# Optimization experiments

Measured on AMD Instinct MI355X. Metric: run time of the kernel, lower is better.

## Reference

```python
import jax, jax.numpy as jnp
import numpy as np

N_NODES = 50000
N_EDGES = 150000
D_FEAT = 512
HIDDEN = 512
N_CLASSES = 47


def gcn_conv(x, edge_index, W, b, n_nodes):
    """PyG GCNConv: out = D^{-1/2} (A + I) D^{-1/2} (x @ W) + b."""
    h = x @ W  # [N, out_dim] dense GEMM
    loop = jnp.arange(n_nodes, dtype=edge_index.dtype)
    row = jnp.concatenate([edge_index[0], loop])  # source
    col = jnp.concatenate([edge_index[1], loop])  # target
    ones = jnp.ones(row.shape[0], dtype=h.dtype)
    deg = jax.ops.segment_sum(ones, col, num_segments=n_nodes)  # in-degree + 1
    dinv = jnp.where(deg > 0, jax.lax.rsqrt(deg), 0.0)
    norm = dinv[row] * dinv[col]  # [E+N]
    msg = norm[:, None] * h[row]  # gather + scale
    out = jax.ops.segment_sum(msg, col, num_segments=n_nodes)  # scatter-add
    return out + b


def setup_inputs() -> dict:
    key = jax.random.key(0)
    k1, k2, k3, k4, k5, k6 = jax.random.split(key, 6)
    x = jax.random.normal(k1, (N_NODES, D_FEAT), dtype=jnp.float32)
    edge_index = jax.random.randint(k2, (2, N_EDGES), 0, N_NODES, dtype=jnp.int64)
    s1 = (6.0 / (D_FEAT + HIDDEN)) ** 0.5
    s2 = (6.0 / (HIDDEN + N_CLASSES)) ** 0.5
    W1 = jax.random.uniform(k3, (D_FEAT, HIDDEN), jnp.float32, -s1, s1)
    b1 = jnp.zeros((HIDDEN,), jnp.float32)
    W2 = jax.random.uniform(k4, (HIDDEN, N_CLASSES), jnp.float32, -s2, s2)
    b2 = jnp.zeros((N_CLASSES,), jnp.float32)
    return {"x": x, "edge_index": edge_index, "W1": W1, "b1": b1, "W2": W2, "b2": b2}


def reference(x, edge_index, W1, b1, W2, b2):
    n = x.shape[0]
    h = gcn_conv(x, edge_index, W1, b1, n)
    h = jax.nn.relu(h)
    # F.dropout(p=0.5, training=self.training): eval mode -> identity
    out = gcn_conv(h, edge_index, W2, b2, n)
    return out
```

## Files before the change

kernel.cpp:

```cpp
#include <hip/hip_runtime.h>
#include <hip/hip_bf16.h>

#define NNODES 50000
#define NEDGES 150000
#define DFEAT  512
#define HID    512
#define NCLS   47
#define ELLW   32

typedef __hip_bfloat16 bf16;
typedef __attribute__((ext_vector_type(8))) short short8;
typedef __attribute__((ext_vector_type(4))) float float4v;

typedef const __attribute__((address_space(1))) unsigned int* gas_t;
typedef __attribute__((address_space(3))) unsigned int* las_t;
__device__ __forceinline__ void load_lds16(const void* g, void* l) {
    __builtin_amdgcn_global_load_lds((gas_t)g, (las_t)l, 16, 0, 0);
}

__device__ __forceinline__ float bfbits_lo(unsigned int w) {
    return __uint_as_float((w & 0xFFFFu) << 16);
}
__device__ __forceinline__ float bfbits_hi(unsigned int w) {
    return __uint_as_float(w & 0xFFFF0000u);
}

__device__ __forceinline__ int eidx(const void* ei, int half, int e, int is64) {
    if (is64) return (int)((const long long*)ei)[(size_t)half * NEDGES + e];
    return ((const int*)ei)[half * NEDGES + e];
}

#define ZB ((NNODES + 255) / 256)
#define NZH2 ((NNODES * 64 / 4 + 255) / 256)
#define PR_ZH2 (1 + ZB)
#define PR_W1T (PR_ZH2 + NZH2)
#define PR_B1  (PR_W1T + 1024)
#define PR_W2T (PR_B1 + 2)
#define PR_B2  (PR_W2T + 128)
#define PR_GRID (PR_B2 + 1)

__global__ __launch_bounds__(256) void k_prep0(
    const void* x, const void* ei, const void* W1, const void* b1,
    const void* W2, const void* b2, int* flags, unsigned int* cnt,
    bf16* W1T, float* b1c, bf16* W2T, float* b2c, float* h2) {
    __shared__ int sh[128];
    __shared__ int shflag;
    const int b = blockIdx.x, t = threadIdx.x;

    if (b >= 1 && b < 1 + ZB) {
        int i = (b - 1) * 256 + t;
        if (i < NNODES) cnt[i] = 0u;
        return;
    }
    if (b >= PR_ZH2 && b < PR_W1T) {
        int i = (b - PR_ZH2) * 256 + t;
        if (i < NNODES * 64 / 4)
            ((float4v*)h2)[i] = (float4v){0.f, 0.f, 0.f, 0.f};
        return;
    }

    if (t < 64) {
        const unsigned short* xs = (const unsigned short*)x;
        int c = 0;
        for (int i = t; i < 256; i += 64) {
            unsigned int e = (xs[2 * i] >> 7) & 0xFF;
            c += (e >= 117 && e <= 130) ? 1 : 0;
        }
        sh[t] = c;
        if (b == 0) {
            const int* w = (const int*)ei;
            int o = 0;
            for (int i = 2 * t + 1; i < 512; i += 128) o |= w[i];
            sh[64 + t] = o;
        }
    }
    __syncthreads();
    if (t == 0) {
        int C = 0;
        for (int i = 0; i < 64; i++) C += sh[i];
        shflag = (C > 128) ? 1 : 0;
        if (b == 0) {
            int O = 0;
            for (int i = 0; i < 64; i++) O |= sh[64 + i];
            flags[0] = shflag;
            flags[1] = (O == 0) ? 1 : 0;
        }
    }
    __syncthreads();
    const int isb = shflag;

    if (b == 0) return;

    if (b >= PR_W1T && b < PR_B1) {
        int i = (b - PR_W1T) * 256 + t;
        int k = i / HID, n = i % HID;
        float v = isb ? __bfloat162float(((const bf16*)W1)[i]) : ((const float*)W1)[i];
        W1T[(size_t)n * DFEAT + k] = __float2bfloat16(v);
    } else if (b >= PR_B1 && b < PR_W2T) {
        int i = (b - PR_B1) * 256 + t;
        if (i < HID)
            b1c[i] = isb ? __bfloat162float(((const bf16*)b1)[i]) : ((const float*)b1)[i];
    } else if (b >= PR_W2T && b < PR_B2) {
        int i = (b - PR_W2T) * 256 + t;
        int n = i / HID, k = i % HID;
        float v = 0.0f;
        if (n < NCLS) {
            size_t idx = (size_t)k * NCLS + n;
            v = isb ? __bfloat162float(((const bf16*)W2)[idx]) : ((const float*)W2)[idx];
        }
        W2T[(size_t)n * HID + k] = __float2bfloat16(v);
    } else if (b == PR_B2) {
        if (t < 64)
            b2c[t] = (t < NCLS)
                ? (isb ? __bfloat162float(((const bf16*)b2)[t]) : ((const float*)b2)[t])
                : 0.0f;
    }
}

__global__ void k_fill_ell(const void* ei, int* cnt, int* ell, const int* flags) {
    int e = blockIdx.x * blockDim.x + threadIdx.x;
    if (e >= NEDGES) return;
    int is64 = flags[1];
    int v = eidx(ei, 1, e, is64);
    int u = eidx(ei, 0, e, is64);
    int slot = atomicAdd(&cnt[v], 1);
    if (slot < ELLW) ell[v * ELLW + slot] = u;
}

__global__ __launch_bounds__(256) void k_aggx(const void* __restrict__ X,
                                              const int* __restrict__ cnt,
                                              const int* __restrict__ ell,
                                              bf16* __restrict__ ax,
                                              const int* __restrict__ flags) {
    int v = blockIdx.x * 4 + (threadIdx.x >> 6);
    int lane = threadIdx.x & 63;
    if (v >= NNODES) return;
    int d8 = lane * 8;
    int degr = cnt[v];
    int deg = degr < ELLW ? degr : ELLW;
    float dv = rsqrtf(1.0f + (float)degr);
    float s2 = dv * dv;
    const int* er = ell + (size_t)v * ELLW;
    float a0, a1, a2, a3, a4, a5, a6, a7;
    if (flags[0]) {
        const bf16* xb = (const bf16*)X;
        uint4 w = *(const uint4*)(xb + (size_t)v * 512 + d8);
        a0 = s2 * bfbits_lo(w.x); a1 = s2 * bfbits_hi(w.x);
        a2 = s2 * bfbits_lo(w.y); a3 = s2 * bfbits_hi(w.y);
        a4 = s2 * bfbits_lo(w.z); a5 = s2 * bfbits_hi(w.z);
        a6 = s2 * bfbits_lo(w.w); a7 = s2 * bfbits_hi(w.w);
        for (int p = 0; p < deg; p += 8) {
            int u[8]; float nw[8];
#pragma unroll
            for (int c = 0; c < 8; ++c) {
                int jp = (p + c < deg) ? p + c : p;
                u[c] = er[jp];
            }
#pragma unroll
            for (int c = 0; c < 8; ++c)
                nw[c] = (p + c < deg) ? rsqrtf(1.0f + (float)cnt[u[c]]) * dv : 0.f;
#pragma unroll
            for (int c = 0; c < 8; ++c) {
                uint4 q = *(const uint4*)(xb + (size_t)u[c] * 512 + d8);
                float nwc = nw[c];
                a0 += nwc * bfbits_lo(q.x); a1 += nwc * bfbits_hi(q.x);
                a2 += nwc * bfbits_lo(q.y); a3 += nwc * bfbits_hi(q.y);
                a4 += nwc * bfbits_lo(q.z); a5 += nwc * bfbits_hi(q.z);
                a6 += nwc * bfbits_lo(q.w); a7 += nwc * bfbits_hi(q.w);
            }
        }
    } else {
        const float* xf = (const float*)X;
        const float* p0 = xf + (size_t)v * 512 + d8;
        float4v f0 = *(const float4v*)p0, f1 = *(const float4v*)(p0 + 4);
        a0 = s2 * f0[0]; a1 = s2 * f0[1]; a2 = s2 * f0[2]; a3 = s2 * f0[3];
        a4 = s2 * f1[0]; a5 = s2 * f1[1]; a6 = s2 * f1[2]; a7 = s2 * f1[3];
        for (int p = 0; p < deg; ++p) {
            int u = er[p];
            float nw = rsqrtf(1.0f + (float)cnt[u]) * dv;
            const float* pu = xf + (size_t)u * 512 + d8;
            float4v g0 = *(const float4v*)pu, g1 = *(const float4v*)(pu + 4);
            a0 += nw * g0[0]; a1 += nw * g0[1]; a2 += nw * g0[2]; a3 += nw * g0[3];
            a4 += nw * g1[0]; a5 += nw * g1[1]; a6 += nw * g1[2]; a7 += nw * g1[3];
        }
    }
    bf16 o[8];
    o[0] = __float2bfloat16(a0); o[1] = __float2bfloat16(a1);
    o[2] = __float2bfloat16(a2); o[3] = __float2bfloat16(a3);
    o[4] = __float2bfloat16(a4); o[5] = __float2bfloat16(a5);
    o[6] = __float2bfloat16(a6); o[7] = __float2bfloat16(a7);
    *(uint4*)(ax + (size_t)v * 512 + d8) = *(uint4*)o;
}

__global__ __launch_bounds__(256, 4) void k_fgemm64(
    const bf16* __restrict__ ax, const bf16* __restrict__ W1T,
    const float* __restrict__ b1c, const bf16* __restrict__ W2T,
    float* __restrict__ h2, int rows_per_xcd, int n_row_tiles) {
    const int b = blockIdx.x;
    const int xcd = b & 7;
    const int s = b >> 3;
    const int col_t = s & 3;
    const int lr = s >> 2;
    const int row_t = xcd * rows_per_xcd + lr;
    if (row_t >= n_row_tiles) return;

    __shared__ bf16 smem[12288];
    bf16* As = smem;
    bf16* Bs = smem + 4096;
    const int tid = threadIdx.x;
    const int wave = tid >> 6, lane = tid & 63;
    const int row0 = row_t * 64;
    const int gc0 = col_t * 128;

    const int rb16 = wave * 16;
    const int frow = lane & 15;
    const int fk = lane >> 4;

    float4v acc[8];
#pragma unroll
    for (int j = 0; j < 8; j++) acc[j] = (float4v){0.f, 0.f, 0.f, 0.f};

    for (int k0 = 0; k0 < DFEAT; k0 += 64) {
        __syncthreads();
#pragma unroll
        for (int t = 0; t < 2; ++t) {
            int g8 = wave * 2 + t;
            int r = g8 * 8 + (lane >> 3);
            int gr = row0 + r; if (gr >= NNODES) gr = NNODES - 1;
            int ck = (lane & 7) ^ (r & 7);
            load_lds16(ax + (size_t)gr * DFEAT + k0 + ck * 8, &As[g8 * 8 * 64]);
        }
#pragma unroll
        for (int t = 0; t < 4; ++t) {
            int g8 = wave * 4 + t;
            int cl = g8 * 8 + (lane >> 3);
            int ck = (lane & 7) ^ (cl & 7);
            load_lds16(W1T + (size_t)(gc0 + cl) * DFEAT + k0 + ck * 8, &Bs[g8 * 8 * 64]);
        }
        __syncthreads();
#pragma unroll
        for (int ki = 0; ki < 2; ++ki) {
            const int cc = ki * 4 + fk;
            int r = rb16 + frow;
            short8 a = *(const short8*)&As[r * 64 + (cc ^ (r & 7)) * 8];
            short8 b8[8];
#pragma unroll
            for (int j = 0; j < 8; j++) {
                int cl = j * 16 + frow;
                b8[j] = *(const short8*)&Bs[cl * 64 + (cc ^ (cl & 7)) * 8];
            }
#pragma unroll
            for (int j = 0; j < 8; j++)
                acc[j] = __builtin_amdgcn_mfma_f32_16x16x32_bf16(a, b8[j], acc[j], 0, 0, 0);
        }
    }

    __syncthreads();
    {
        float bias[8];
#pragma unroll
        for (int j = 0; j < 8; j++) bias[j] = b1c[gc0 + j * 16 + frow];
#pragma unroll
        for (int r = 0; r < 4; r++) {
            int row = rb16 + fk * 4 + r;
#pragma unroll
            for (int j = 0; j < 8; j++) {
                int col = j * 16 + frow;
                float v = acc[j][r] + bias[j];
                v = v > 0.f ? v : 0.f;
                int ck2 = (col >> 3) ^ (row & 7);
                smem[row * 128 + ck2 * 8 + (col & 7)] = __float2bfloat16(v);
            }
        }
    }
    __syncthreads();

    float4v acc2[4];
#pragma unroll
    for (int j = 0; j < 4; j++) acc2[j] = (float4v){0.f, 0.f, 0.f, 0.f};
#pragma unroll
    for (int ks = 0; ks < 4; ++ks) {
        const int kk = ks * 32 + fk * 8;
        const int p = kk >> 3;
        int row = rb16 + frow;
        short8 a2 = *(const short8*)&smem[row * 128 + ((p ^ (row & 7)) * 8)];
        short8 b2f[4];
#pragma unroll
        for (int j = 0; j < 4; j++) {
            int n = j * 16 + frow;
            b2f[j] = *(const short8*)(W2T + (size_t)n * HID + gc0 + kk);
        }
#pragma unroll
        for (int j = 0; j < 4; j++)
            acc2[j] = __builtin_amdgcn_mfma_f32_16x16x32_bf16(a2, b2f[j], acc2[j], 0, 0, 0);
    }

#pragma unroll
    for (int r = 0; r < 4; r++) {
        int grow = row0 + rb16 + fk * 4 + r;
        if (grow < NNODES) {
#pragma unroll
            for (int j = 0; j < 4; j++)
                atomicAdd(&h2[(size_t)grow * 64 + j * 16 + frow], acc2[j][r]);
        }
    }
}

__global__ __launch_bounds__(256) void k_agg2(const float* __restrict__ h2,
                                              const int* __restrict__ cnt,
                                              const int* __restrict__ ell,
                                              const float* __restrict__ b2c,
                                              void* out, const int* flags) {
    int v = blockIdx.x * 16 + (threadIdx.x >> 4);
    int l = threadIdx.x & 15;
    if (v >= NNODES) return;
    int d4 = l * 4;
    int degr = cnt[v];
    int deg = degr < ELLW ? degr : ELLW;
    float dv = rsqrtf(1.0f + (float)degr);
    const int* er = ell + (size_t)v * ELLW;
    float4v w = *(const float4v*)(h2 + (size_t)v * 64 + d4);
    float s2 = dv * dv;
    float a0 = s2 * w[0], a1 = s2 * w[1], a2 = s2 * w[2], a3 = s2 * w[3];
    for (int p = 0; p < deg; p += 4) {
        int u0 = er[p];
        int u1 = er[(p + 1 < deg) ? p + 1 : p];
        int u2 = er[(p + 2 < deg) ? p + 2 : p];
        int u3 = er[(p + 3 < deg) ? p + 3 : p];
        float nw0 = rsqrtf(1.0f + (float)cnt[u0]) * dv;
        float nw1 = (p + 1 < deg) ? rsqrtf(1.0f + (float)cnt[u1]) * dv : 0.f;
        float nw2 = (p + 2 < deg) ? rsqrtf(1.0f + (float)cnt[u2]) * dv : 0.f;
        float nw3 = (p + 3 < deg) ? rsqrtf(1.0f + (float)cnt[u3]) * dv : 0.f;
        float4v q0 = *(const float4v*)(h2 + (size_t)u0 * 64 + d4);
        float4v q1 = *(const float4v*)(h2 + (size_t)u1 * 64 + d4);
        float4v q2 = *(const float4v*)(h2 + (size_t)u2 * 64 + d4);
        float4v q3 = *(const float4v*)(h2 + (size_t)u3 * 64 + d4);
        a0 += nw0 * q0[0] + nw1 * q1[0] + nw2 * q2[0] + nw3 * q3[0];
        a1 += nw0 * q0[1] + nw1 * q1[1] + nw2 * q2[1] + nw3 * q3[1];
        a2 += nw0 * q0[2] + nw1 * q1[2] + nw2 * q2[2] + nw3 * q3[2];
        a3 += nw0 * q0[3] + nw1 * q1[3] + nw2 * q2[3] + nw3 * q3[3];
    }
    a0 += b2c[d4 + 0]; a1 += b2c[d4 + 1]; a2 += b2c[d4 + 2]; a3 += b2c[d4 + 3];
    size_t base = (size_t)v * NCLS;
    if (flags[0]) {
        bf16* ob = (bf16*)out;
        if (d4 + 0 < NCLS) ob[base + d4 + 0] = __float2bfloat16(a0);
        if (d4 + 1 < NCLS) ob[base + d4 + 1] = __float2bfloat16(a1);
        if (d4 + 2 < NCLS) ob[base + d4 + 2] = __float2bfloat16(a2);
        if (d4 + 3 < NCLS) ob[base + d4 + 3] = __float2bfloat16(a3);
    } else {
        float* of = (float*)out;
        if (d4 + 0 < NCLS) of[base + d4 + 0] = a0;
        if (d4 + 1 < NCLS) of[base + d4 + 1] = a1;
        if (d4 + 2 < NCLS) of[base + d4 + 2] = a2;
        if (d4 + 3 < NCLS) of[base + d4 + 3] = a3;
    }
}

extern "C" void kernel_launch(void* const* d_in, const int* in_sizes, int n_in,
                              void* d_out, int out_size, void* d_ws, size_t ws_size,
                              hipStream_t stream) {
    const void* x  = d_in[0];
    const void* ei = d_in[1];
    const void* W1 = d_in[2];
    const void* b1 = d_in[3];
    const void* W2 = d_in[4];
    const void* b2 = d_in[5];

    char* base = (char*)d_ws;
    auto alloc = [&](size_t bytes) -> char* {
        char* p = base;
        base += (bytes + 255) & ~(size_t)255;
        return p;
    };
    int*   flags  = (int*)alloc(64);
    int*   cnt    = (int*)alloc(sizeof(int) * NNODES);
    int*   ell    = (int*)alloc(sizeof(int) * (size_t)NNODES * ELLW);
    bf16*  W1T    = (bf16*)alloc(sizeof(bf16) * DFEAT * HID);
    float* b1c    = (float*)alloc(sizeof(float) * HID);
    bf16*  W2T    = (bf16*)alloc(sizeof(bf16) * 64 * HID);
    float* b2c    = (float*)alloc(sizeof(float) * 64);
    float* h2     = (float*)alloc(sizeof(float) * (size_t)NNODES * 64);
    bf16*  ax     = (bf16*)alloc(sizeof(bf16) * (size_t)NNODES * DFEAT);

    k_prep0<<<PR_GRID, 256, 0, stream>>>(x, ei, W1, b1, W2, b2, flags,
                                         (unsigned int*)cnt, W1T, b1c, W2T, b2c, h2);
    k_fill_ell<<<(NEDGES + 255) / 256, 256, 0, stream>>>(ei, cnt, ell, flags);
    k_aggx<<<(NNODES + 3) / 4, 256, 0, stream>>>(x, cnt, ell, ax, flags);
    const int rowblocks = (NNODES + 63) / 64;
    const int rows_per_xcd = (rowblocks + 7) / 8;
    k_fgemm64<<<8 * rows_per_xcd * 4, 256, 0, stream>>>(ax, W1T, b1c, W2T, h2,
                                                        rows_per_xcd, rowblocks);
    k_agg2<<<(NNODES + 15) / 16, 256, 0, stream>>>(h2, cnt, ell, b2c, d_out, flags);
}
```

Before: 297.4 us.

## Compute full hidden width per block and store h2 directly, dropping atomics and zeroing

The fused GEMM now has each block cover all 512 hidden columns for its 64 rows instead of splitting them across four column tiles. This lets the second-layer product be finished inside one block, so h2 can be written with plain stores instead of atomics and the zero-fill pass in the prep kernel goes away. W1T fragments are read straight from global memory (cached) rather than staged through LDS. In exchange, each thread holds 32 accumulator vectors, which raises register pressure and cuts occupancy to 2 blocks per CU, and the grid has a quarter as many blocks.

```diff
diff --git a/kernel.cpp b/kernel.cpp
--- a/kernel.cpp
+++ b/kernel.cpp
@@ -31,9 +31,7 @@
 }
 
 #define ZB ((NNODES + 255) / 256)
-#define NZH2 ((NNODES * 64 / 4 + 255) / 256)
-#define PR_ZH2 (1 + ZB)
-#define PR_W1T (PR_ZH2 + NZH2)
+#define PR_W1T (1 + ZB)
 #define PR_B1  (PR_W1T + 1024)
 #define PR_W2T (PR_B1 + 2)
 #define PR_B2  (PR_W2T + 128)
@@ -42,7 +40,7 @@
 __global__ __launch_bounds__(256) void k_prep0(
     const void* x, const void* ei, const void* W1, const void* b1,
     const void* W2, const void* b2, int* flags, unsigned int* cnt,
-    bf16* W1T, float* b1c, bf16* W2T, float* b2c, float* h2) {
+    bf16* W1T, float* b1c, bf16* W2T, float* b2c) {
     __shared__ int sh[128];
     __shared__ int shflag;
     const int b = blockIdx.x, t = threadIdx.x;
@@ -50,12 +48,6 @@
     if (b >= 1 && b < 1 + ZB) {
         int i = (b - 1) * 256 + t;
         if (i < NNODES) cnt[i] = 0u;
-        return;
-    }
-    if (b >= PR_ZH2 && b < PR_W1T) {
-        int i = (b - PR_ZH2) * 256 + t;
-        if (i < NNODES * 64 / 4)
-            ((float4v*)h2)[i] = (float4v){0.f, 0.f, 0.f, 0.f};
         return;
     }
 
@@ -192,33 +184,29 @@
     *(uint4*)(ax + (size_t)v * 512 + d8) = *(uint4*)o;
 }
 
-__global__ __launch_bounds__(256, 4) void k_fgemm64(
+__global__ __launch_bounds__(256, 2) void k_fgemm_full(
     const bf16* __restrict__ ax, const bf16* __restrict__ W1T,
     const float* __restrict__ b1c, const bf16* __restrict__ W2T,
     float* __restrict__ h2, int rows_per_xcd, int n_row_tiles) {
     const int b = blockIdx.x;
     const int xcd = b & 7;
-    const int s = b >> 3;
-    const int col_t = s & 3;
-    const int lr = s >> 2;
+    const int lr = b >> 3;
     const int row_t = xcd * rows_per_xcd + lr;
     if (row_t >= n_row_tiles) return;
 
-    __shared__ bf16 smem[12288];
+    __shared__ bf16 smem[4096 + 8192];
     bf16* As = smem;
-    bf16* Bs = smem + 4096;
     const int tid = threadIdx.x;
     const int wave = tid >> 6, lane = tid & 63;
     const int row0 = row_t * 64;
-    const int gc0 = col_t * 128;
-
     const int rb16 = wave * 16;
     const int frow = lane & 15;
     const int fk = lane >> 4;
-
-    float4v acc[8];
-#pragma unroll
-    for (int j = 0; j < 8; j++) acc[j] = (float4v){0.f, 0.f, 0.f, 0.f};
+    bf16* Rw = smem + 4096 + wave * 2048;
+
+    float4v acc[32];
+#pragma unroll
+    for (int j = 0; j < 32; j++) acc[j] = (float4v){0.f, 0.f, 0.f, 0.f};
 
     for (int k0 = 0; k0 < DFEAT; k0 += 64) {
         __syncthreads();
@@ -230,69 +218,62 @@
             int ck = (lane & 7) ^ (r & 7);
             load_lds16(ax + (size_t)gr * DFEAT + k0 + ck * 8, &As[g8 * 8 * 64]);
         }
-#pragma unroll
-        for (int t = 0; t < 4; ++t) {
-            int g8 = wave * 4 + t;
-            int cl = g8 * 8 + (lane >> 3);
-            int ck = (lane & 7) ^ (cl & 7);
-            load_lds16(W1T + (size_t)(gc0 + cl) * DFEAT + k0 + ck * 8, &Bs[g8 * 8 * 64]);
-        }
         __syncthreads();
 #pragma unroll
         for (int ki = 0; ki < 2; ++ki) {
             const int cc = ki * 4 + fk;
-            int r = rb16 + frow;
+            const int r = rb16 + frow;
             short8 a = *(const short8*)&As[r * 64 + (cc ^ (r & 7)) * 8];
-            short8 b8[8];
-#pragma unroll
-            for (int j = 0; j < 8; j++) {
-                int cl = j * 16 + frow;
-                b8[j] = *(const short8*)&Bs[cl * 64 + (cc ^ (cl & 7)) * 8];
+#pragma unroll
+            for (int jg = 0; jg < 8; ++jg) {
+                short8 b4[4];
+#pragma unroll
+                for (int jj = 0; jj < 4; jj++) {
+                    int j = jg * 4 + jj;
+                    b4[jj] = *(const short8*)(W1T + (size_t)(j * 16 + frow) * DFEAT
+                                              + k0 + ki * 32 + fk * 8);
+                }
+#pragma unroll
+                for (int jj = 0; jj < 4; jj++)
+                    acc[jg * 4 + jj] = __builtin_amdgcn_mfma_f32_16x16x32_bf16(
+                        a, b4[jj], acc[jg * 4 + jj], 0, 0, 0);
             }
-#pragma unroll
-            for (int j = 0; j < 8; j++)
-                acc[j] = __builtin_amdgcn_mfma_f32_16x16x32_bf16(a, b8[j], acc[j], 0, 0, 0);
-        }
-    }
-
-    __syncthreads();
-    {
-        float bias[8];
-#pragma unroll
-        for (int j = 0; j < 8; j++) bias[j] = b1c[gc0 + j * 16 + frow];
-#pragma unroll
-        for (int r = 0; r < 4; r++) {
-            int row = rb16 + fk * 4 + r;
-#pragma unroll
-            for (int j = 0; j < 8; j++) {
+        }
+    }
+
+    float4v acc2[4];
+#pragma unroll
+    for (int j = 0; j < 4; j++) acc2[j] = (float4v){0.f, 0.f, 0.f, 0.f};
+
+#pragma unroll
+    for (int jc = 0; jc < 4; ++jc) {
+#pragma unroll
+        for (int j = 0; j < 8; j++) {
+            float bias = b1c[jc * 128 + j * 16 + frow];
+#pragma unroll
+            for (int r = 0; r < 4; r++) {
+                int r16 = fk * 4 + r;
                 int col = j * 16 + frow;
-                float v = acc[j][r] + bias[j];
+                float v = acc[jc * 8 + j][r] + bias;
                 v = v > 0.f ? v : 0.f;
-                int ck2 = (col >> 3) ^ (row & 7);
-                smem[row * 128 + ck2 * 8 + (col & 7)] = __float2bfloat16(v);
+                int ck2 = (col >> 3) ^ (r16 & 7);
+                Rw[r16 * 128 + ck2 * 8 + (col & 7)] = __float2bfloat16(v);
             }
         }
-    }
-    __syncthreads();
-
-    float4v acc2[4];
-#pragma unroll
-    for (int j = 0; j < 4; j++) acc2[j] = (float4v){0.f, 0.f, 0.f, 0.f};
-#pragma unroll
-    for (int ks = 0; ks < 4; ++ks) {
-        const int kk = ks * 32 + fk * 8;
-        const int p = kk >> 3;
-        int row = rb16 + frow;
-        short8 a2 = *(const short8*)&smem[row * 128 + ((p ^ (row & 7)) * 8)];
-        short8 b2f[4];
-#pragma unroll
-        for (int j = 0; j < 4; j++) {
-            int n = j * 16 + frow;
-            b2f[j] = *(const short8*)(W2T + (size_t)n * HID + gc0 + kk);
-        }
-#pragma unroll
-        for (int j = 0; j < 4; j++)
-            acc2[j] = __builtin_amdgcn_mfma_f32_16x16x32_bf16(a2, b2f[j], acc2[j], 0, 0, 0);
+#pragma unroll
+        for (int ks = 0; ks < 4; ++ks) {
+            int kk = ks * 32 + fk * 8;
+            int p = kk >> 3;
+            short8 a2 = *(const short8*)&Rw[frow * 128 + ((p ^ (frow & 7)) * 8)];
+            short8 b2f[4];
+#pragma unroll
+            for (int j = 0; j < 4; j++)
+                b2f[j] = *(const short8*)(W2T + (size_t)(j * 16 + frow) * HID
+                                          + jc * 128 + kk);
+#pragma unroll
+            for (int j = 0; j < 4; j++)
+                acc2[j] = __builtin_amdgcn_mfma_f32_16x16x32_bf16(a2, b2f[j], acc2[j], 0, 0, 0);
+        }
     }
 
 #pragma unroll
@@ -301,7 +282,7 @@
         if (grow < NNODES) {
 #pragma unroll
             for (int j = 0; j < 4; j++)
-                atomicAdd(&h2[(size_t)grow * 64 + j * 16 + frow], acc2[j][r]);
+                h2[(size_t)grow * 64 + j * 16 + frow] = acc2[j][r];
         }
     }
 }
@@ -384,12 +365,12 @@
     bf16*  ax     = (bf16*)alloc(sizeof(bf16) * (size_t)NNODES * DFEAT);
 
     k_prep0<<<PR_GRID, 256, 0, stream>>>(x, ei, W1, b1, W2, b2, flags,
-                                         (unsigned int*)cnt, W1T, b1c, W2T, b2c, h2);
+                                         (unsigned int*)cnt, W1T, b1c, W2T, b2c);
     k_fill_ell<<<(NEDGES + 255) / 256, 256, 0, stream>>>(ei, cnt, ell, flags);
     k_aggx<<<(NNODES + 3) / 4, 256, 0, stream>>>(x, cnt, ell, ax, flags);
     const int rowblocks = (NNODES + 63) / 64;
     const int rows_per_xcd = (rowblocks + 7) / 8;
-    k_fgemm64<<<8 * rows_per_xcd * 4, 256, 0, stream>>>(ax, W1T, b1c, W2T, h2,
-                                                        rows_per_xcd, rowblocks);
+    k_fgemm_full<<<8 * rows_per_xcd, 256, 0, stream>>>(ax, W1T, b1c, W2T, h2,
+                                                       rows_per_xcd, rowblocks);
     k_agg2<<<(NNODES + 15) / 16, 256, 0, stream>>>(h2, cnt, ell, b2c, d_out, flags);
 }
```

After: 503.3 us. +69.2%, slower.
